# Performance work log

Hardware: AMD Instinct MI355X
Metric: run time of the kernel (lower is better)

## Reference

```python
import jax, jax.numpy as jnp
import numpy as np

B, T, N, IN = 16, 12, 2048, 1
HID, E_DIM, CHEB, HOR = 64, 10, 2, 12


def setup_inputs() -> dict:
    key = jax.random.key(0)
    ks = jax.random.split(key, 12)
    s = 0.1  # param scale to keep gates unsaturated
    return {
        "source": jax.random.normal(ks[0], (B, T, N, IN), jnp.float32),
        "node_embeddings": jax.random.normal(ks[1], (N, E_DIM), jnp.float32),
        "Wg0": jax.random.normal(ks[2], (E_DIM, CHEB, IN + HID, 2 * HID), jnp.float32) * s,
        "bg0": jax.random.normal(ks[3], (E_DIM, 2 * HID), jnp.float32) * s,
        "Wu0": jax.random.normal(ks[4], (E_DIM, CHEB, IN + HID, HID), jnp.float32) * s,
        "bu0": jax.random.normal(ks[5], (E_DIM, HID), jnp.float32) * s,
        "Wg1": jax.random.normal(ks[6], (E_DIM, CHEB, HID + HID, 2 * HID), jnp.float32) * s,
        "bg1": jax.random.normal(ks[7], (E_DIM, 2 * HID), jnp.float32) * s,
        "Wu1": jax.random.normal(ks[8], (E_DIM, CHEB, HID + HID, HID), jnp.float32) * s,
        "bu1": jax.random.normal(ks[9], (E_DIM, HID), jnp.float32) * s,
        "conv_w": jax.random.normal(ks[10], (HOR, HID), jnp.float32) * s,
        "conv_b": jax.random.normal(ks[11], (HOR,), jnp.float32) * s,
    }


def _cheb_supports(E, cheb_k):
    # softmax(relu(E E^T)) row-normalized adaptive adjacency + Chebyshev recursion
    S = jax.nn.softmax(jax.nn.relu(E @ E.T), axis=1)
    sup = [jnp.eye(E.shape[0], dtype=S.dtype), S]
    for _ in range(2, cheb_k):
        sup.append(2.0 * S @ sup[-1] - sup[-2])
    return jnp.stack(sup, axis=0)  # (K, N, N)


def _gcn(x, supports, weights, bias):
    # x: (B,N,C); weights: (N,K,C,O); bias: (N,O)
    x_g = jnp.einsum('knm,bmc->bnkc', supports, x)
    return jnp.einsum('bnki,nkio->bno', x_g, weights) + bias


def _layer(x_seq, supports, E, Wg, bg, Wu, bu, hid):
    # precompute node-adaptive weights/biases (constant across time)
    wg = jnp.einsum('nd,dkio->nkio', E, Wg)
    bgv = E @ bg
    wu = jnp.einsum('nd,dkio->nkio', E, Wu)
    buv = E @ bu

    def step(state, x_t):
        inp = jnp.concatenate([x_t, state], axis=-1)
        zr = jax.nn.sigmoid(_gcn(inp, supports, wg, bgv))
        z, r = jnp.split(zr, 2, axis=-1)
        cand = jnp.concatenate([x_t, z * state], axis=-1)
        hc = jnp.tanh(_gcn(cand, supports, wu, buv))
        h = r * state + (1.0 - r) * hc
        return h, h

    init = jnp.zeros((x_seq.shape[0], x_seq.shape[2], hid), dtype=x_seq.dtype)
    _, hs = jax.lax.scan(step, init, jnp.swapaxes(x_seq, 0, 1))  # (T,B,N,H)
    return jnp.swapaxes(hs, 0, 1)  # (B,T,N,H)


def reference(source, node_embeddings, Wg0, bg0, Wu0, bu0, Wg1, bg1, Wu1, bu1, conv_w, conv_b):
    supports = _cheb_supports(node_embeddings, CHEB)
    h1 = _layer(source, supports, node_embeddings, Wg0, bg0, Wu0, bu0, HID)
    h2 = _layer(h1, supports, node_embeddings, Wg1, bg1, Wu1, bu1, HID)
    last = h2[:, -1]  # (B,N,HID)
    # Conv2d(1, horizon, kernel=(1,HID)) on (B,1,N,HID) == per-node linear over HID
    out = jnp.einsum('bnc,hc->bhn', last, conv_w) + conv_b[None, :, None]
    return out  # (B, horizon, N)
```

## Files before the change

kernel.cpp:

```cpp
#include <hip/hip_runtime.h>
#include <hip/hip_bf16.h>


#define B_    16
#define T_    12
#define N_    2048
#define HID_  64
#define ED_   10
#define HOR_  12
#define BH    (B_*HID_)
#define BT    (B_*T_)

typedef __hip_bfloat16 bf16;
typedef __attribute__((ext_vector_type(8))) short short8;
typedef __attribute__((ext_vector_type(4))) float floatx4;

__device__ __forceinline__ float b2f(bf16 x){ return __bfloat162float(x); }
__device__ __forceinline__ bf16  f2b(float x){ return __float2bfloat16(x); }
__device__ __forceinline__ float bits2f(unsigned u) {
  union { float f; unsigned i; } c; c.i = u << 16; return c.f;
}
__device__ __forceinline__ float ldin(const void* p, size_t i, int isbf) {
  return isbf ? b2f(((const bf16*)p)[i]) : ((const float*)p)[i];
}
__device__ __forceinline__ void fma4(float4& a, float s, const float4& b) {
  a.x += s*b.x; a.y += s*b.y; a.z += s*b.z; a.w += s*b.w;
}

__global__ void k_detect(const void* __restrict__ E, int* __restrict__ flag) {
  __shared__ int cnt;
  if (threadIdx.x == 0) cnt = 0;
  __syncthreads();
  const unsigned* w = (const unsigned*)E;
  int c = 0;
  for (int i = threadIdx.x; i < 4096; i += 256) {
    const unsigned e = (w[i] >> 7) & 0xFFu;
    if (e >= 0x6Eu && e <= 0x86u) ++c;
  }
  atomicAdd(&cnt, c);
  __syncthreads();
  if (threadIdx.x == 0) flag[0] = (cnt > 2048) ? 1 : 0;
}

__global__ void k_castE(const void* __restrict__ E, float* __restrict__ Ein,
                        const int* __restrict__ flag) {
  const int i = blockIdx.x*256 + threadIdx.x;
  if (i < N_*ED_) Ein[i] = ldin(E, i, flag[0]);
}
__global__ void k_castsrc(const void* __restrict__ src, float* __restrict__ srcf,
                          const int* __restrict__ flag) {
  const int i = blockIdx.x*256 + threadIdx.x;
  if (i < B_*T_*N_) srcf[i] = ldin(src, i, flag[0]);
}
__global__ void k_castc(const void* __restrict__ cw, const void* __restrict__ cb,
                        float* __restrict__ cwf, float* __restrict__ cbf,
                        const int* __restrict__ flag) {
  const int i = blockIdx.x*256 + threadIdx.x;
  const int f = flag[0];
  if (i < HOR_*HID_) cwf[i] = ldin(cw, i, f);
  if (i < HOR_)      cbf[i] = ldin(cb, i, f);
}

__global__ __launch_bounds__(256) void k_softmax_S(const float* __restrict__ Ein,
                                                   float* __restrict__ S) {
  const int n = blockIdx.x, tid = threadIdx.x;
  __shared__ float er[ED_];
  __shared__ float red[4];
  if (tid < ED_) er[tid] = Ein[n*ED_ + tid];
  __syncthreads();
  float e[ED_];
#pragma unroll
  for (int d = 0; d < ED_; ++d) e[d] = er[d];
  float v[8];
  float mx = 0.f;
#pragma unroll
  for (int j = 0; j < 8; ++j) {
    const int m = tid + j*256;
    float dot = 0.f;
#pragma unroll
    for (int d = 0; d < ED_; ++d) dot += e[d]*Ein[m*ED_ + d];
    v[j] = fmaxf(dot, 0.f);
    mx = fmaxf(mx, v[j]);
  }
  for (int o = 32; o; o >>= 1) mx = fmaxf(mx, __shfl_xor(mx, o, 64));
  if ((tid & 63) == 0) red[tid >> 6] = mx;
  __syncthreads();
  mx = fmaxf(fmaxf(red[0], red[1]), fmaxf(red[2], red[3]));
  __syncthreads();
  float sum = 0.f;
#pragma unroll
  for (int j = 0; j < 8; ++j) { v[j] = __expf(v[j] - mx); sum += v[j]; }
  for (int o = 32; o; o >>= 1) sum += __shfl_xor(sum, o, 64);
  if ((tid & 63) == 0) red[tid >> 6] = sum;
  __syncthreads();
  sum = red[0] + red[1] + red[2] + red[3];
  const float inv = 1.f / sum;
#pragma unroll
  for (int j = 0; j < 8; ++j)
    S[(size_t)n*N_ + tid + j*256] = v[j]*inv;
}

__global__ void k_splitS(const float* __restrict__ S, bf16* __restrict__ Sh,
                         bf16* __restrict__ Sl, int n) {
  const int i = blockIdx.x*256 + threadIdx.x;
  if (i < n) {
    const float v = S[i];
    const bf16 h = f2b(v);
    Sh[i] = h;
    Sl[i] = f2b(v - b2f(h));
  }
}

__global__ __launch_bounds__(256) void k_trsp(const float* __restrict__ X,
                                              bf16* __restrict__ Th,
                                              bf16* __restrict__ Tl) {
  const int n0 = blockIdx.x * 64;
  const int c0 = blockIdx.y * 64;
  __shared__ float t[64][68];
  const int tid = threadIdx.x;
  {
    const int r = tid >> 2, q4 = (tid & 3) * 16;
    const float4* src = (const float4*)(X + (size_t)(n0 + r)*BH + c0 + q4);
#pragma unroll
    for (int u = 0; u < 4; ++u)
      *(float4*)&t[r][q4 + u*4] = src[u];
  }
  __syncthreads();
  {
    const int c = tid >> 2, sg = (tid & 3) * 16;
    bf16 hb[16], lb[16];
#pragma unroll
    for (int i = 0; i < 16; ++i) {
      const float v = t[sg + i][c];
      const bf16 h = f2b(v);
      hb[i] = h;
      lb[i] = f2b(v - b2f(h));
    }
    bf16* dh = Th + (size_t)(c0 + c)*N_ + n0 + sg;
    bf16* dl = Tl + (size_t)(c0 + c)*N_ + n0 + sg;
    *(uint4*)dh       = *(uint4*)&hb[0];
    *(uint4*)(dh + 8) = *(uint4*)&hb[8];
    *(uint4*)dl       = *(uint4*)&lb[0];
    *(uint4*)(dl + 8) = *(uint4*)&lb[8];
  }
}

template<int LAYER>
__global__ __launch_bounds__(256) void k_prepP(const void* __restrict__ Wb,
                                               float* __restrict__ PF,
                                               bf16* __restrict__ PH,
                                               int KIin, int KIP, int O,
                                               const int* __restrict__ flag) {
  const int idx = blockIdx.x*256 + threadIdx.x;
  if (idx >= ED_*O*KIP) return;
  const int d = idx / (O*KIP), rem = idx - d*O*KIP;
  const int o = rem / KIP, kp = rem - o*KIP;
  int cheb, i; bool valid;
  if (LAYER == 0) {
    cheb = (kp >= 80) ? 1 : 0;
    const int local = kp - cheb*80;
    if (local < 64)       { i = local + 1; valid = true; }
    else if (local == 64) { i = 0;         valid = true; }
    else                  { i = 0;         valid = false; }
  } else {
    cheb = kp >> 7; i = kp & 127; valid = true;
  }
  float v = 0.f;
  if (valid) v = ldin(Wb, (size_t)((d*2 + cheb)*KIin + i)*O + o, flag[0]);
  const int kg = kp >> 2, e = kp & 3;
  const size_t pi = ((size_t)(o*(KIP/4) + kg)*ED_ + d)*4 + e;
  PF[pi] = v;
  PH[pi] = f2b(v);
}

__global__ __launch_bounds__(128) void k_matb(const float* __restrict__ Ein,
                                              const void* __restrict__ bb,
                                              float* __restrict__ outv, int O,
                                              const int* __restrict__ flag) {
  const int n = blockIdx.x, tid = threadIdx.x;
  if (tid >= O) return;
  const int f = flag[0];
  float acc = 0.f;
#pragma unroll
  for (int d = 0; d < ED_; ++d) acc += Ein[n*ED_ + d]*ldin(bb, d*O + tid, f);
  outv[n*O + tid] = acc;
}

__global__ __launch_bounds__(256) void k_gemm64T(const float* __restrict__ S,
                                                 const float* __restrict__ X,
                                                 float* __restrict__ C,
                                                 int ldx, int ldc) {
  const int bm = blockIdx.x * 64;
  const int bc = blockIdx.y * 64;
  __shared__ float St[64][68];
  __shared__ float Xt[64][68];
  const int tid = threadIdx.x;
  const int r0 = (tid >> 4) * 4;
  const int c0 = (tid & 15) * 4;
  float acc[4][4];
#pragma unroll
  for (int i = 0; i < 4; ++i)
#pragma unroll
    for (int j = 0; j < 4; ++j) acc[i][j] = 0.f;
  for (int mk = 0; mk < N_; mk += 64) {
    {
      const int r = tid >> 2, ks = (tid & 3) * 16;
      const float* sp = S + (size_t)(bm + r)*N_ + mk + ks;
#pragma unroll
      for (int u = 0; u < 16; ++u) St[ks + u][r] = sp[u];
      const float* xp = X + (size_t)(bc + r)*ldx + mk + ks;
#pragma unroll
      for (int u = 0; u < 16; ++u) Xt[ks + u][r] = xp[u];
    }
    __syncthreads();
#pragma unroll 4
    for (int kk = 0; kk < 64; ++kk) {
      const float a0 = St[kk][r0], a1 = St[kk][r0+1],
                  a2 = St[kk][r0+2], a3 = St[kk][r0+3];
      const float b0 = Xt[kk][c0], b1 = Xt[kk][c0+1],
                  b2 = Xt[kk][c0+2], b3 = Xt[kk][c0+3];
      acc[0][0] += a0*b0; acc[0][1] += a0*b1; acc[0][2] += a0*b2; acc[0][3] += a0*b3;
      acc[1][0] += a1*b0; acc[1][1] += a1*b1; acc[1][2] += a1*b2; acc[1][3] += a1*b3;
      acc[2][0] += a2*b0; acc[2][1] += a2*b1; acc[2][2] += a2*b2; acc[2][3] += a2*b3;
      acc[3][0] += a3*b0; acc[3][1] += a3*b1; acc[3][2] += a3*b2; acc[3][3] += a3*b3;
    }
    __syncthreads();
  }
#pragma unroll
  for (int i = 0; i < 4; ++i)
#pragma unroll
    for (int j = 0; j < 4; ++j)
      C[(size_t)(bm + r0 + i)*ldc + bc + c0 + j] = acc[i][j];
}

__global__ __launch_bounds__(256) void k_gemmM(const bf16* __restrict__ Sh,
                                               const bf16* __restrict__ Sl,
                                               const bf16* __restrict__ X1h,
                                               const bf16* __restrict__ X1l,
                                               float* __restrict__ C1, int ldc1,
                                               const bf16* __restrict__ X2h,
                                               const bf16* __restrict__ X2l,
                                               float* __restrict__ C2, int ldc2,
                                               int split) {
  const int bm = blockIdx.x * 128;
  int bc = blockIdx.y * 64;
  const bf16* Xh = X1h; const bf16* Xl = X1l; float* C = C1; int ldc = ldc1;
  if (bc >= split) { Xh = X2h; Xl = X2l; C = C2; ldc = ldc2; bc -= split; }

  __shared__ __align__(16) bf16 Ah[128][72];
  __shared__ __align__(16) bf16 Al[128][72];
  __shared__ __align__(16) bf16 Bh[64][72];
  __shared__ __align__(16) bf16 Bl[64][72];
  const int tid = threadIdx.x;
  const int wave = tid >> 6, lane = tid & 63, q = lane >> 4, ln = lane & 15;
  const int wm = wave >> 1, wn = wave & 1;
  const int srow = tid >> 3, scol = (tid & 7) * 8;

  floatx4 acc[4][2];
#pragma unroll
  for (int mt = 0; mt < 4; ++mt)
#pragma unroll
    for (int nt = 0; nt < 2; ++nt) acc[mt][nt] = (floatx4){0.f,0.f,0.f,0.f};

  for (int mk = 0; mk < N_; mk += 64) {
#pragma unroll
    for (int i = 0; i < 4; ++i) {
      const int r = i*32 + srow;
      *(uint4*)&Ah[r][scol] = *(const uint4*)(Sh + (size_t)(bm + r)*N_ + mk + scol);
      *(uint4*)&Al[r][scol] = *(const uint4*)(Sl + (size_t)(bm + r)*N_ + mk + scol);
    }
#pragma unroll
    for (int i = 0; i < 2; ++i) {
      const int r = i*32 + srow;
      *(uint4*)&Bh[r][scol] = *(const uint4*)(Xh + (size_t)(bc + r)*N_ + mk + scol);
      *(uint4*)&Bl[r][scol] = *(const uint4*)(Xl + (size_t)(bc + r)*N_ + mk + scol);
    }
    __syncthreads();
#pragma unroll
    for (int ks = 0; ks < 64; ks += 32) {
      short8 ah[4], al[4], bh[2], bl[2];
#pragma unroll
      for (int mt = 0; mt < 4; ++mt) {
        ah[mt] = *(const short8*)&Ah[wm*64 + mt*16 + ln][ks + q*8];
        al[mt] = *(const short8*)&Al[wm*64 + mt*16 + ln][ks + q*8];
      }
#pragma unroll
      for (int nt = 0; nt < 2; ++nt) {
        bh[nt] = *(const short8*)&Bh[wn*32 + nt*16 + ln][ks + q*8];
        bl[nt] = *(const short8*)&Bl[wn*32 + nt*16 + ln][ks + q*8];
      }
#pragma unroll
      for (int mt = 0; mt < 4; ++mt)
#pragma unroll
        for (int nt = 0; nt < 2; ++nt) {
          acc[mt][nt] = __builtin_amdgcn_mfma_f32_16x16x32_bf16(ah[mt], bh[nt], acc[mt][nt], 0, 0, 0);
          acc[mt][nt] = __builtin_amdgcn_mfma_f32_16x16x32_bf16(al[mt], bh[nt], acc[mt][nt], 0, 0, 0);
          acc[mt][nt] = __builtin_amdgcn_mfma_f32_16x16x32_bf16(ah[mt], bl[nt], acc[mt][nt], 0, 0, 0);
        }
    }
    __syncthreads();
  }
#pragma unroll
  for (int mt = 0; mt < 4; ++mt)
#pragma unroll
    for (int nt = 0; nt < 2; ++nt)
#pragma unroll
      for (int r = 0; r < 4; ++r)
        C[(size_t)(bm + wm*64 + mt*16 + q*4 + r)*ldc + bc + wn*32 + nt*16 + ln] =
            acc[mt][nt][r];
}

template<int LAYER, int KIP, int KIPP>
__device__ __forceinline__ void build4(float (*xg)[KIPP],
                                       const float* p0, const float* p1,
                                       const float* p2, const float* p3,
                                       int n, int t, int tid) {
  constexpr int NQ = KIP/4;
  for (int idx = tid; idx < B_*NQ; idx += 256) {
    const int b = idx / NQ, k = (idx - b*NQ) * 4;
    float4 v = make_float4(0.f, 0.f, 0.f, 0.f);
    if (LAYER == 1) {
      const float* rg = (k < 64) ? p0 : (k < 128) ? p1 : (k < 192) ? p2 : p3;
      v = *(const float4*)(rg + (size_t)n*BH + b*64 + (k & 63));
    } else {
      if (k < 64)        v = *(const float4*)(p0 + (size_t)n*BH + b*64 + k);
      else if (k == 64)  v.x = p1[(size_t)(b*T_ + t)*N_ + n];
      else if (k >= 80 && k < 144)
                         v = *(const float4*)(p2 + (size_t)n*BH + b*64 + (k - 80));
      else if (k == 144) v.x = p3[(size_t)n*BT + b*T_ + t];
    }
    *(float4*)&xg[b][k] = v;
  }
}

template<int KIP>
__device__ __forceinline__ float4 merge_p(const float* __restrict__ PF,
                                          const bf16* __restrict__ PH,
                                          const float* el, int o, int kg,
                                          int isbf) {
  float4 a4 = make_float4(0.f, 0.f, 0.f, 0.f);
  const size_t gbase = (size_t)(o*(KIP/4) + kg)*(ED_*4);
  if (isbf) {
    const uint4* g = (const uint4*)(PH + gbase);
#pragma unroll
    for (int i = 0; i < 5; ++i) {
      const uint4 w = g[i];
      const float e0 = el[2*i], e1 = el[2*i + 1];
      a4.x += e0*bits2f(w.x & 0xFFFFu); a4.y += e0*bits2f(w.x >> 16);
      a4.z += e0*bits2f(w.y & 0xFFFFu); a4.w += e0*bits2f(w.y >> 16);
      a4.x += e1*bits2f(w.z & 0xFFFFu); a4.y += e1*bits2f(w.z >> 16);
      a4.z += e1*bits2f(w.w & 0xFFFFu); a4.w += e1*bits2f(w.w >> 16);
    }
  } else {
    const float4* g = (const float4*)(PF + gbase);
#pragma unroll
    for (int d = 0; d < ED_; ++d)
      fma4(a4, el[d], g[d]);
  }
  return a4;
}

template<int KIP>
__device__ __forceinline__ void merge_p2(const float* __restrict__ PF,
                                         const bf16* __restrict__ PH,
                                         const float* el0, const float* el1,
                                         int o, int kg, int isbf,
                                         float4& a0, float4& a1) {
  const size_t gbase = (size_t)(o*(KIP/4) + kg)*(ED_*4);
  if (isbf) {
    const uint4* g = (const uint4*)(PH + gbase);
#pragma unroll
    for (int i = 0; i < 5; ++i) {
      const uint4 w = g[i];
      const float f0 = bits2f(w.x & 0xFFFFu), f1 = bits2f(w.x >> 16);
      const float f2 = bits2f(w.y & 0xFFFFu), f3 = bits2f(w.y >> 16);
      const float f4 = bits2f(w.z & 0xFFFFu), f5 = bits2f(w.z >> 16);
      const float f6 = bits2f(w.w & 0xFFFFu), f7 = bits2f(w.w >> 16);
      const float e00 = el0[2*i], e01 = el0[2*i + 1];
      const float e10 = el1[2*i], e11 = el1[2*i + 1];
      a0.x += e00*f0; a0.y += e00*f1; a0.z += e00*f2; a0.w += e00*f3;
      a0.x += e01*f4; a0.y += e01*f5; a0.z += e01*f6; a0.w += e01*f7;
      a1.x += e10*f0; a1.y += e10*f1; a1.z += e10*f2; a1.w += e10*f3;
      a1.x += e11*f4; a1.y += e11*f5; a1.z += e11*f6; a1.w += e11*f7;
    }
  } else {
    const float4* g = (const float4*)(PF + gbase);
#pragma unroll
    for (int d = 0; d < ED_; ++d) {
      const float4 w = g[d];
      fma4(a0, el0[d], w);
      fma4(a1, el1[d], w);
    }
  }
}

template<int KIP>
__global__ __launch_bounds__(256) void k_merge(const float* __restrict__ PF,
                                               const bf16* __restrict__ PH,
                                               const float* __restrict__ Ein,
                                               float* __restrict__ WM, int O,
                                               const int* __restrict__ flag) {
  const int n = blockIdx.x;
  const int idx = blockIdx.y*256 + threadIdx.x;
  __shared__ float es[ED_];
  if (threadIdx.x < ED_) es[threadIdx.x] = Ein[n*ED_ + threadIdx.x];
  __syncthreads();
  if (idx >= O*(KIP/4)) return;
  const int o = idx / (KIP/4), kg = idx - o*(KIP/4);
  float el[ED_];
#pragma unroll
  for (int d = 0; d < ED_; ++d) el[d] = es[d];
  const float4 a4 = merge_p<KIP>(PF, PH, el, o, kg, flag[0]);
  *(float4*)&WM[((size_t)n*O + o)*KIP + kg*4] = a4;
}

template<int LAYER, int KIP>
__global__ __launch_bounds__(256, 2) void k_gateWpm(const float* __restrict__ WM,
                                                    const float* __restrict__ bgv,
                                                    const float* __restrict__ p0,
                                                    const float* __restrict__ p1,
                                                    const float* __restrict__ p2,
                                                    const float* __restrict__ p3,
                                                    const float* __restrict__ hstate,
                                                    float* __restrict__ zh,
                                                    float* __restrict__ r_buf,
                                                    int t) {
  constexpr int KIPP = KIP + 4;
  constexpr int O = 128;
  const int n = blockIdx.x, tid = threadIdx.x;
  __shared__ float xg[B_][KIPP];
  __shared__ float wm[O][36];
  build4<LAYER, KIP, KIPP>(xg, p0, p1, p2, p3, n, t, tid);

  const float* WMn = WM + (size_t)n*O*KIP;
  const int b = tid >> 4, q = tid & 15;
  float acc[8];
#pragma unroll
  for (int j = 0; j < 8; ++j) acc[j] = 0.f;

  for (int k0 = 0; k0 < KIP; k0 += 32) {
#pragma unroll
    for (int i = 0; i < O*8/256; ++i) {
      const int idx = tid + i*256;
      const int o = idx >> 3, kq = idx & 7;
      *(float4*)&wm[o][kq*4] =
          *(const float4*)(WMn + (size_t)o*KIP + k0 + kq*4);
    }
    __syncthreads();
#pragma unroll
    for (int kq = 0; kq < 8; ++kq) {
      const float4 xv = *(const float4*)&xg[b][k0 + kq*4];
#pragma unroll
      for (int j = 0; j < 8; ++j) {
        const float4 wv = *(const float4*)&wm[q + 16*j][kq*4];
        acc[j] += xv.x*wv.x + xv.y*wv.y + xv.z*wv.z + xv.w*wv.w;
      }
    }
    __syncthreads();
  }
#pragma unroll
  for (int j = 0; j < 8; ++j) {
    const int o = q + 16*j;
    float s = acc[j] + bgv[n*128 + o];
    s = 1.f/(1.f + __expf(-s));
    if (o < HID_) {
      const float zv = s*hstate[(size_t)n*BH + b*64 + o];
      zh[(size_t)n*BH + b*64 + o] = zv;
    } else {
      r_buf[(size_t)n*BH + b*64 + (o - HID_)] = s;
    }
  }
}

template<int LAYER, int KIP>
__global__ __launch_bounds__(256, 2) void k_candWpm(const float* __restrict__ WM,
                                                    const float* __restrict__ buv,
                                                    const float* __restrict__ p0,
                                                    const float* __restrict__ p1,
                                                    const float* __restrict__ p2,
                                                    const float* __restrict__ p3,
                                                    const float* __restrict__ r_buf,
                                                    float* __restrict__ hstate,
                                                    int t) {
  constexpr int KIPP = KIP + 4;
  constexpr int O = 64;
  const int n = blockIdx.x, tid = threadIdx.x;
  __shared__ float xg[B_][KIPP];
  __shared__ float wm[O][36];
  build4<LAYER, KIP, KIPP>(xg, p0, p1, p2, p3, n, t, tid);

  const float* WMn = WM + (size_t)n*O*KIP;
  const int b = tid >> 4, q = tid & 15;
  float acc[4];
#pragma unroll
  for (int j = 0; j < 4; ++j) acc[j] = 0.f;

  for (int k0 = 0; k0 < KIP; k0 += 32) {
#pragma unroll
    for (int i = 0; i < O*8/256; ++i) {
      const int idx = tid + i*256;
      const int o = idx >> 3, kq = idx & 7;
      *(float4*)&wm[o][kq*4] =
          *(const float4*)(WMn + (size_t)o*KIP + k0 + kq*4);
    }
    __syncthreads();
#pragma unroll
    for (int kq = 0; kq < 8; ++kq) {
      const float4 xv = *(const float4*)&xg[b][k0 + kq*4];
#pragma unroll
      for (int j = 0; j < 4; ++j) {
        const float4 wv = *(const float4*)&wm[q + 16*j][kq*4];
        acc[j] += xv.x*wv.x + xv.y*wv.y + xv.z*wv.z + xv.w*wv.w;
      }
    }
    __syncthreads();
  }
#pragma unroll
  for (int j = 0; j < 4; ++j) {
    const int o = q + 16*j;
    const float hc = tanhf(acc[j] + buv[n*64 + o]);
    const float rr = r_buf[(size_t)n*BH + b*64 + o];
    const float hold = hstate[(size_t)n*BH + b*64 + o];
    const float hn = rr*hold + (1.f - rr)*hc;
    hstate[(size_t)n*BH + b*64 + o] = hn;
  }
}

template<int LAYER, int KIP>
__global__ __launch_bounds__(256, 2) void k_gateW2(const float* __restrict__ PF,
                                                   const bf16* __restrict__ PH,
                                                   const float* __restrict__ bgv,
                                                   const float* __restrict__ p0,
                                                   const float* __restrict__ p1,
                                                   const float* __restrict__ p2,
                                                   const float* __restrict__ p3,
                                                   const float* __restrict__ Ein,
                                                   const float* __restrict__ hstate,
                                                   float* __restrict__ zh,
                                                   float* __restrict__ r_buf,
                                                   const int* __restrict__ flag,
                                                   int t) {
  constexpr int KIPP = KIP + 4;
  constexpr int O = 128;
  const int n0 = blockIdx.x, n1 = blockIdx.x + N_/2, tid = threadIdx.x;
  __shared__ float xg[2][B_][KIPP];
  __shared__ float wm[2][O][36];
  __shared__ float es[2][ED_];
  if (tid < ED_) es[0][tid] = Ein[n0*ED_ + tid];
  if (tid >= 32 && tid < 32 + ED_) es[1][tid - 32] = Ein[n1*ED_ + (tid - 32)];
  build4<LAYER, KIP, KIPP>(xg[0], p0, p1, p2, p3, n0, t, tid);
  build4<LAYER, KIP, KIPP>(xg[1], p0, p1, p2, p3, n1, t, tid);
  __syncthreads();
  const int isbf = flag[0];
  float el0[ED_], el1[ED_];
#pragma unroll
  for (int d = 0; d < ED_; ++d) { el0[d] = es[0][d]; el1[d] = es[1][d]; }

  const int b = tid >> 4, q = tid & 15;
  float ac0[8], ac1[8];
#pragma unroll
  for (int j = 0; j < 8; ++j) { ac0[j] = 0.f; ac1[j] = 0.f; }

  for (int k0 = 0; k0 < KIP; k0 += 32) {
#pragma unroll
    for (int i = 0; i < O*8/256; ++i) {
      const int idx = tid + i*256;
      const int o = idx >> 3, kq = idx & 7;
      float4 a0 = make_float4(0.f, 0.f, 0.f, 0.f);
      float4 a1 = make_float4(0.f, 0.f, 0.f, 0.f);
      merge_p2<KIP>(PF, PH, el0, el1, o, (k0 >> 2) + kq, isbf, a0, a1);
      *(float4*)&wm[0][o][kq*4] = a0;
      *(float4*)&wm[1][o][kq*4] = a1;
    }
    __syncthreads();
#pragma unroll
    for (int kq = 0; kq < 8; ++kq) {
      const float4 xv0 = *(const float4*)&xg[0][b][k0 + kq*4];
      const float4 xv1 = *(const float4*)&xg[1][b][k0 + kq*4];
#pragma unroll
      for (int j = 0; j < 8; ++j) {
        const float4 w0 = *(const float4*)&wm[0][q + 16*j][kq*4];
        const float4 w1 = *(const float4*)&wm[1][q + 16*j][kq*4];
        ac0[j] += xv0.x*w0.x + xv0.y*w0.y + xv0.z*w0.z + xv0.w*w0.w;
        ac1[j] += xv1.x*w1.x + xv1.y*w1.y + xv1.z*w1.z + xv1.w*w1.w;
      }
    }
    __syncthreads();
  }
#pragma unroll
  for (int j = 0; j < 8; ++j) {
    const int o = q + 16*j;
    {
      float s = ac0[j] + bgv[n0*128 + o];
      s = 1.f/(1.f + __expf(-s));
      if (o < HID_) {
        zh[(size_t)n0*BH + b*64 + o] = s*hstate[(size_t)n0*BH + b*64 + o];
      } else {
        r_buf[(size_t)n0*BH + b*64 + (o - HID_)] = s;
      }
    }
    {
      float s = ac1[j] + bgv[n1*128 + o];
      s = 1.f/(1.f + __expf(-s));
      if (o < HID_) {
        zh[(size_t)n1*BH + b*64 + o] = s*hstate[(size_t)n1*BH + b*64 + o];
      } else {
        r_buf[(size_t)n1*BH + b*64 + (o - HID_)] = s;
      }
    }
  }
}

template<int LAYER, int KIP>
__global__ __launch_bounds__(256, 2) void k_candW2f(const float* __restrict__ PF,
                                                    const bf16* __restrict__ PH,
                                                    const float* __restrict__ buv,
                                                    const float* __restrict__ p0,
                                                    const float* __restrict__ p1,
                                                    const float* __restrict__ p2,
                                                    const float* __restrict__ p3,
                                                    const float* __restrict__ Ein,
                                                    const float* __restrict__ r_buf,
                                                    float* __restrict__ hstate,
                                                    const int* __restrict__ flag,
                                                    int t) {
  constexpr int KIPP = KIP + 4;
  constexpr int O = 64;
  const int n0 = blockIdx.x, n1 = blockIdx.x + N_/2, tid = threadIdx.x;
  __shared__ float xg[2][B_][KIPP];
  __shared__ float wm[2][O][36];
  __shared__ float es[2][ED_];
  if (tid < ED_) es[0][tid] = Ein[n0*ED_ + tid];
  if (tid >= 32 && tid < 32 + ED_) es[1][tid - 32] = Ein[n1*ED_ + (tid - 32)];
  build4<LAYER, KIP, KIPP>(xg[0], p0, p1, p2, p3, n0, t, tid);
  build4<LAYER, KIP, KIPP>(xg[1], p0, p1, p2, p3, n1, t, tid);
  __syncthreads();
  const int isbf = flag[0];
  float el0[ED_], el1[ED_];
#pragma unroll
  for (int d = 0; d < ED_; ++d) { el0[d] = es[0][d]; el1[d] = es[1][d]; }

  const int b = tid >> 4, q = tid & 15;
  float ac0[4], ac1[4];
#pragma unroll
  for (int j = 0; j < 4; ++j) { ac0[j] = 0.f; ac1[j] = 0.f; }

  for (int k0 = 0; k0 < KIP; k0 += 32) {
#pragma unroll
    for (int i = 0; i < O*8/256; ++i) {
      const int idx = tid + i*256;
      const int o = idx >> 3, kq = idx & 7;
      float4 a0 = make_float4(0.f, 0.f, 0.f, 0.f);
      float4 a1 = make_float4(0.f, 0.f, 0.f, 0.f);
      merge_p2<KIP>(PF, PH, el0, el1, o, (k0 >> 2) + kq, isbf, a0, a1);
      *(float4*)&wm[0][o][kq*4] = a0;
      *(float4*)&wm[1][o][kq*4] = a1;
    }
    __syncthreads();
#pragma unroll
    for (int kq = 0; kq < 8; ++kq) {
      const float4 xv0 = *(const float4*)&xg[0][b][k0 + kq*4];
      const float4 xv1 = *(const float4*)&xg[1][b][k0 + kq*4];
#pragma unroll
      for (int j = 0; j < 4; ++j) {
        const float4 w0 = *(const float4*)&wm[0][q + 16*j][kq*4];
        const float4 w1 = *(const float4*)&wm[1][q + 16*j][kq*4];
        ac0[j] += xv0.x*w0.x + xv0.y*w0.y + xv0.z*w0.z + xv0.w*w0.w;
        ac1[j] += xv1.x*w1.x + xv1.y*w1.y + xv1.z*w1.z + xv1.w*w1.w;
      }
    }
    __syncthreads();
  }
#pragma unroll
  for (int j = 0; j < 4; ++j) {
    const int o = q + 16*j;
    {
      const float hc = tanhf(ac0[j] + buv[n0*64 + o]);
      const float rr = r_buf[(size_t)n0*BH + b*64 + o];
      const float hold = hstate[(size_t)n0*BH + b*64 + o];
      hstate[(size_t)n0*BH + b*64 + o] = rr*hold + (1.f - rr)*hc;
    }
    {
      const float hc = tanhf(ac1[j] + buv[n1*64 + o]);
      const float rr = r_buf[(size_t)n1*BH + b*64 + o];
      const float hold = hstate[(size_t)n1*BH + b*64 + o];
      hstate[(size_t)n1*BH + b*64 + o] = rr*hold + (1.f - rr)*hc;
    }
  }
}

__global__ void k_zero_f(float* __restrict__ p, int n) {
  const int i = blockIdx.x*256 + threadIdx.x;
  if (i < n) p[i] = 0.f;
}
__global__ void k_zero_out(void* __restrict__ out, int nelem,
                           const int* __restrict__ flag) {
  const int i = blockIdx.x*256 + threadIdx.x;
  if (i < nelem) {
    if (flag[0]) ((unsigned short*)out)[i] = 0;
    else         ((float*)out)[i] = 0.f;
  }
}

__global__ __launch_bounds__(256) void k_conv(const float* __restrict__ h2,
                                              const float* __restrict__ cwf,
                                              const float* __restrict__ cbf,
                                              void* __restrict__ out,
                                              const int* __restrict__ flag) {
  const int n = blockIdx.x, tid = threadIdx.x;
  __shared__ float hs[BH];
  for (int i = tid; i < BH; i += 256) hs[i] = h2[(size_t)n*BH + i];
  __syncthreads();
  const int isbf = flag[0];
  for (int i = tid; i < B_*HOR_; i += 256) {
    const int b = i / HOR_, hor = i - b*HOR_;
    float acc = cbf[hor];
#pragma unroll
    for (int c = 0; c < HID_; ++c) acc += hs[b*HID_ + c]*cwf[hor*HID_ + c];
    const size_t oi = (size_t)(b*HOR_ + hor)*N_ + n;
    if (isbf) ((bf16*)out)[oi] = f2b(acc);
    else      ((float*)out)[oi] = acc;
  }
}

extern "C" void kernel_launch(void* const* d_in, const int* in_sizes, int n_in,
                              void* d_out, int out_size, void* d_ws, size_t ws_size,
                              hipStream_t stream) {
  const void* src = d_in[0];
  const void* E   = d_in[1];
  const void* Wg0 = d_in[2];
  const void* bg0 = d_in[3];
  const void* Wu0 = d_in[4];
  const void* bu0 = d_in[5];
  const void* Wg1 = d_in[6];
  const void* bg1 = d_in[7];
  const void* Wu1 = d_in[8];
  const void* bu1 = d_in[9];
  const void* cw  = d_in[10];
  const void* cb  = d_in[11];
  (void)in_sizes; (void)n_in;

  char* p = (char*)d_ws;
  char* ws_end = (char*)d_ws + ws_size;
  auto alloc = [&](size_t bytes) -> char* {
    char* r = p; p += (bytes + 255) & ~(size_t)255; return r;
  };
  const size_t SL = (size_t)N_*BH;
  int*   flag  = (int*)  alloc(256);
  float* Ein   = (float*)alloc((size_t)N_*ED_*4);
  float* cwf   = (float*)alloc((size_t)HOR_*HID_*4);
  float* cbf   = (float*)alloc((size_t)HOR_*4);
  float* S_f   = (float*)alloc((size_t)N_*N_*4);
  bf16*  S_hi  = (bf16*) alloc((size_t)N_*N_*2);
  bf16*  S_lo  = (bf16*) alloc((size_t)N_*N_*2);
  float* Wg0F  = (float*)alloc((size_t)ED_*128*160*4);
  float* Wu0F  = (float*)alloc((size_t)ED_*64*160*4);
  float* Wg1F  = (float*)alloc((size_t)ED_*128*256*4);
  float* Wu1F  = (float*)alloc((size_t)ED_*64*256*4);
  bf16*  Wg0H  = (bf16*) alloc((size_t)ED_*128*160*2);
  bf16*  Wu0H  = (bf16*) alloc((size_t)ED_*64*160*2);
  bf16*  Wg1H  = (bf16*) alloc((size_t)ED_*128*256*2);
  bf16*  Wu1H  = (bf16*) alloc((size_t)ED_*64*256*2);
  float* bgv0  = (float*)alloc((size_t)N_*128*4);
  float* buv0  = (float*)alloc((size_t)N_*64*4);
  float* bgv1  = (float*)alloc((size_t)N_*128*4);
  float* buv1  = (float*)alloc((size_t)N_*64*4);
  float* srcf  = (float*)alloc((size_t)BT*N_*4);
  float* Sx0   = (float*)alloc((size_t)N_*BT*4);
  float* h0    = (float*)alloc(SL*4);
  float* h2    = (float*)alloc(SL*4);
  float* Sh_a  = (float*)alloc(SL*4);
  float* Sh_b  = (float*)alloc(SL*4);
  float* zh    = (float*)alloc(SL*4);
  float* r_buf = (float*)alloc(SL*4);
  bf16*  zhTh  = (bf16*) alloc(SL*2);
  bf16*  zhTl  = (bf16*) alloc(SL*2);
  bf16*  h0Th  = (bf16*) alloc(SL*2);
  bf16*  h0Tl  = (bf16*) alloc(SL*2);
  bf16*  h2Th  = (bf16*) alloc(SL*2);
  bf16*  h2Tl  = (bf16*) alloc(SL*2);

  const size_t required_base = (size_t)(p - (char*)d_ws);

  float* Wu0M = (float*)alloc((size_t)N_*64*160*4);   bool pmWu0 = (p <= ws_end);
  float* Wu1M = (float*)alloc((size_t)N_*64*256*4);   bool pmWu1 = (p <= ws_end);
  float* Wg0M = (float*)alloc((size_t)N_*128*160*4);  bool pmWg0 = (p <= ws_end);
  float* Wg1M = (float*)alloc((size_t)N_*128*256*4);  bool pmWg1 = (p <= ws_end);

  auto cdiv = [](int a, int b) { return (a + b - 1) / b; };

  k_detect<<<dim3(1), 256, 0, stream>>>(E, flag);

  if (required_base > ws_size) {
    k_zero_out<<<dim3(cdiv(out_size, 256)), 256, 0, stream>>>(d_out, out_size, flag);
    return;
  }

  k_castE  <<<dim3(cdiv(N_*ED_, 256)), 256, 0, stream>>>(E, Ein, flag);
  k_castsrc<<<dim3(cdiv(BT*N_, 256)),  256, 0, stream>>>(src, srcf, flag);
  k_castc  <<<dim3(cdiv(HOR_*HID_, 256)), 256, 0, stream>>>(cw, cb, cwf, cbf, flag);
  k_prepP<0><<<dim3(cdiv(ED_*128*160, 256)), 256, 0, stream>>>(Wg0, Wg0F, Wg0H, 65, 160, 128, flag);
  k_prepP<0><<<dim3(cdiv(ED_*64*160,  256)), 256, 0, stream>>>(Wu0, Wu0F, Wu0H, 65, 160, 64, flag);
  k_prepP<1><<<dim3(cdiv(ED_*128*256, 256)), 256, 0, stream>>>(Wg1, Wg1F, Wg1H, 128, 256, 128, flag);
  k_prepP<1><<<dim3(cdiv(ED_*64*256,  256)), 256, 0, stream>>>(Wu1, Wu1F, Wu1H, 128, 256, 64, flag);
  k_matb<<<dim3(N_), 128, 0, stream>>>(Ein, bg0, bgv0, 128, flag);
  k_matb<<<dim3(N_), 128, 0, stream>>>(Ein, bu0, buv0, 64,  flag);
  k_matb<<<dim3(N_), 128, 0, stream>>>(Ein, bg1, bgv1, 128, flag);
  k_matb<<<dim3(N_), 128, 0, stream>>>(Ein, bu1, buv1, 64,  flag);
  k_softmax_S<<<dim3(N_), 256, 0, stream>>>(Ein, S_f);
  k_splitS<<<dim3(cdiv(N_*N_, 256)), 256, 0, stream>>>(S_f, S_hi, S_lo, N_*N_);

  if (pmWu0) k_merge<160><<<dim3(N_, 10), 256, 0, stream>>>(Wu0F, Wu0H, Ein, Wu0M, 64,  flag);
  if (pmWu1) k_merge<256><<<dim3(N_, 16), 256, 0, stream>>>(Wu1F, Wu1H, Ein, Wu1M, 64,  flag);
  if (pmWg0) k_merge<160><<<dim3(N_, 20), 256, 0, stream>>>(Wg0F, Wg0H, Ein, Wg0M, 128, flag);
  if (pmWg1) k_merge<256><<<dim3(N_, 32), 256, 0, stream>>>(Wg1F, Wg1H, Ein, Wg1M, 128, flag);

  k_gemm64T<<<dim3(N_/64, BT/64), 256, 0, stream>>>(S_f, srcf, Sx0, N_, BT);

  k_zero_f<<<dim3((int)((2*SL + 255)/256)), 256, 0, stream>>>(h0, (int)(2*SL));
  k_zero_f<<<dim3((int)((2*SL + 255)/256)), 256, 0, stream>>>(Sh_a, (int)(2*SL));

  auto run_gate0 = [&](int t) {
    if (pmWg0)
      k_gateWpm<0,160><<<dim3(N_), 256, 0, stream>>>(Wg0M, bgv0, h0, srcf, Sh_a, Sx0,
                                                     h0, zh, r_buf, t);
    else
      k_gateW2<0,160><<<dim3(N_/2), 256, 0, stream>>>(Wg0F, Wg0H, bgv0, h0, srcf, Sh_a, Sx0,
                                                      Ein, h0, zh, r_buf, flag, t);
  };
  auto run_cand0 = [&](int t) {
    if (pmWu0)
      k_candWpm<0,160><<<dim3(N_), 256, 0, stream>>>(Wu0M, buv0, zh, srcf, Sh_b, Sx0,
                                                     r_buf, h0, t);
    else
      k_candW2f<0,160><<<dim3(N_/2), 256, 0, stream>>>(Wu0F, Wu0H, buv0, zh, srcf, Sh_b, Sx0,
                                                       Ein, r_buf, h0, flag, t);
  };
  auto run_gate1 = [&](int t) {
    if (pmWg1)
      k_gateWpm<1,256><<<dim3(N_), 256, 0, stream>>>(Wg1M, bgv1, h0, h2, Sh_a, Sh_b,
                                                     h2, zh, r_buf, t);
    else
      k_gateW2<1,256><<<dim3(N_/2), 256, 0, stream>>>(Wg1F, Wg1H, bgv1, h0, h2, Sh_a, Sh_b,
                                                      Ein, h2, zh, r_buf, flag, t);
  };
  auto run_cand1 = [&](int t) {
    if (pmWu1)
      k_candWpm<1,256><<<dim3(N_), 256, 0, stream>>>(Wu1M, buv1, h0, zh, Sh_a, Sh_b,
                                                     r_buf, h2, t);
    else
      k_candW2f<1,256><<<dim3(N_/2), 256, 0, stream>>>(Wu1F, Wu1H, buv1, h0, zh, Sh_a, Sh_b,
                                                       Ein, r_buf, h2, flag, t);
  };
  auto trsp = [&](const float* X, bf16* Th, bf16* Tl) {
    k_trsp<<<dim3(N_/64, BH/64), 256, 0, stream>>>(X, Th, Tl);
  };

  run_gate0(0);
  run_cand0(0);
  trsp(h0, h0Th, h0Tl);
  k_gemmM<<<dim3(N_/128, BH/64), 256, 0, stream>>>(S_hi, S_lo, h0Th, h0Tl, Sh_a, BH,
                                                   h0Th, h0Tl, Sh_a, BH, 1 << 30);
  run_gate1(0);
  run_cand1(0);
  trsp(h2, h2Th, h2Tl);

  for (int t = 1; t < T_; ++t) {
    run_gate0(t);
    trsp(zh, zhTh, zhTl);
    k_gemmM<<<dim3(N_/128, BH/64), 256, 0, stream>>>(S_hi, S_lo, zhTh, zhTl, Sh_b, BH,
                                                     zhTh, zhTl, Sh_b, BH, 1 << 30);
    run_cand0(t);
    trsp(h0, h0Th, h0Tl);
    k_gemmM<<<dim3(N_/128, 2*BH/64), 256, 0, stream>>>(S_hi, S_lo, h0Th, h0Tl, Sh_a, BH,
                                                       h2Th, h2Tl, Sh_b, BH, BH);
    run_gate1(t);
    trsp(zh, zhTh, zhTl);
    k_gemmM<<<dim3(N_/128, BH/64), 256, 0, stream>>>(S_hi, S_lo, zhTh, zhTl, Sh_b, BH,
                                                     zhTh, zhTl, Sh_b, BH, 1 << 30);
    run_cand1(t);
    trsp(h2, h2Th, h2Tl);
  }

  k_conv<<<dim3(N_), 256, 0, stream>>>(h2, cwf, cbf, d_out, flag);
}
```

Baseline: 5.764 ms.

## Move buffers to static device globals and drop premerged-weight and fp32 GEMM paths

Replaces workspace-allocated buffers with statically sized __device__ globals that kernels select by index arguments, so the code no longer depends on workspace size. It drops the per-node premerged-weight kernels (k_merge, k_gateWpm, k_candWpm) and always uses the on-the-fly merge kernels. The fp32 S matrix and its split pass are removed by having softmax write the bf16 hi/lo parts directly. The fp32 source GEMM is replaced with the split-bf16 MFMA GEMM on pre-split source. It also reorders inputs by matching their byte sizes. This avoids the large merged-weight materialization and the separate split pass, but the premerged path may have been faster per step when enough workspace was available.

```diff
diff --git a/kernel.cpp b/kernel.cpp
--- a/kernel.cpp
+++ b/kernel.cpp
@@ -10,10 +10,42 @@
 #define HOR_  12
 #define BH    (B_*HID_)
 #define BT    (B_*T_)
+#define SL_   (N_*BH)
 
 typedef __hip_bfloat16 bf16;
 typedef __attribute__((ext_vector_type(8))) short short8;
 typedef __attribute__((ext_vector_type(4))) float floatx4;
+
+__device__ int            g_flag[64];
+__device__ float          g_Ein[N_*ED_];
+__device__ float          g_cwf[HOR_*HID_];
+__device__ float          g_cbf[HOR_ + 4];
+__device__ unsigned short g_Shi[N_*N_];
+__device__ unsigned short g_Slo[N_*N_];
+__device__ float          g_Wg0F[ED_*128*160];
+__device__ float          g_Wu0F[ED_*64*160];
+__device__ float          g_Wg1F[ED_*128*256];
+__device__ float          g_Wu1F[ED_*64*256];
+__device__ unsigned short g_Wg0H[ED_*128*160];
+__device__ unsigned short g_Wu0H[ED_*64*160];
+__device__ unsigned short g_Wg1H[ED_*128*256];
+__device__ unsigned short g_Wu1H[ED_*64*256];
+__device__ float          g_bgv0[N_*128];
+__device__ float          g_buv0[N_*64];
+__device__ float          g_bgv1[N_*128];
+__device__ float          g_buv1[N_*64];
+__device__ float          g_srcf[BT*N_];
+__device__ unsigned short g_srcHi[BT*N_];
+__device__ unsigned short g_srcLo[BT*N_];
+__device__ float          g_Sx0[N_*BT];
+__device__ float          g_h[2*SL_];
+__device__ float          g_Sh[2*SL_];
+__device__ float          g_zh[SL_];
+__device__ float          g_rbuf[SL_];
+__device__ unsigned short g_tmpTh[SL_];
+__device__ unsigned short g_tmpTl[SL_];
+__device__ unsigned short g_h2Th[SL_];
+__device__ unsigned short g_h2Tl[SL_];
 
 __device__ __forceinline__ float b2f(bf16 x){ return __bfloat162float(x); }
 __device__ __forceinline__ bf16  f2b(float x){ return __float2bfloat16(x); }
@@ -27,7 +59,7 @@
   a.x += s*b.x; a.y += s*b.y; a.z += s*b.z; a.w += s*b.w;
 }
 
-__global__ void k_detect(const void* __restrict__ E, int* __restrict__ flag) {
+__global__ void k_detect(const void* __restrict__ E) {
   __shared__ int cnt;
   if (threadIdx.x == 0) cnt = 0;
   __syncthreads();
@@ -39,34 +71,31 @@
   }
   atomicAdd(&cnt, c);
   __syncthreads();
-  if (threadIdx.x == 0) flag[0] = (cnt > 2048) ? 1 : 0;
-}
-
-__global__ void k_castE(const void* __restrict__ E, float* __restrict__ Ein,
-                        const int* __restrict__ flag) {
+  if (threadIdx.x == 0) g_flag[0] = (cnt > 2048) ? 1 : 0;
+}
+
+__global__ void k_castE(const void* __restrict__ E) {
   const int i = blockIdx.x*256 + threadIdx.x;
-  if (i < N_*ED_) Ein[i] = ldin(E, i, flag[0]);
-}
-__global__ void k_castsrc(const void* __restrict__ src, float* __restrict__ srcf,
-                          const int* __restrict__ flag) {
+  if (i < N_*ED_) g_Ein[i] = ldin(E, i, g_flag[0]);
+}
+__global__ void k_castsrc(const void* __restrict__ src) {
   const int i = blockIdx.x*256 + threadIdx.x;
-  if (i < B_*T_*N_) srcf[i] = ldin(src, i, flag[0]);
-}
-__global__ void k_castc(const void* __restrict__ cw, const void* __restrict__ cb,
-                        float* __restrict__ cwf, float* __restrict__ cbf,
-                        const int* __restrict__ flag) {
+  if (i < B_*T_*N_) g_srcf[i] = ldin(src, i, g_flag[0]);
+}
+__global__ void k_castc(const void* __restrict__ cw, const void* __restrict__ cb) {
   const int i = blockIdx.x*256 + threadIdx.x;
-  const int f = flag[0];
-  if (i < HOR_*HID_) cwf[i] = ldin(cw, i, f);
-  if (i < HOR_)      cbf[i] = ldin(cb, i, f);
-}
-
-__global__ __launch_bounds__(256) void k_softmax_S(const float* __restrict__ Ein,
-                                                   float* __restrict__ S) {
+  const int f = g_flag[0];
+  if (i < HOR_*HID_) g_cwf[i] = ldin(cw, i, f);
+  if (i < HOR_)      g_cbf[i] = ldin(cb, i, f);
+}
+
+__global__ __launch_bounds__(256) void k_softmax_S() {
+  bf16* Sh = (bf16*)g_Shi;
+  bf16* Sl = (bf16*)g_Slo;
   const int n = blockIdx.x, tid = threadIdx.x;
   __shared__ float er[ED_];
   __shared__ float red[4];
-  if (tid < ED_) er[tid] = Ein[n*ED_ + tid];
+  if (tid < ED_) er[tid] = g_Ein[n*ED_ + tid];
   __syncthreads();
   float e[ED_];
 #pragma unroll
@@ -78,7 +107,7 @@
     const int m = tid + j*256;
     float dot = 0.f;
 #pragma unroll
-    for (int d = 0; d < ED_; ++d) dot += e[d]*Ein[m*ED_ + d];
+    for (int d = 0; d < ED_; ++d) dot += e[d]*g_Ein[m*ED_ + d];
     v[j] = fmaxf(dot, 0.f);
     mx = fmaxf(mx, v[j]);
   }
@@ -96,24 +125,29 @@
   sum = red[0] + red[1] + red[2] + red[3];
   const float inv = 1.f / sum;
 #pragma unroll
-  for (int j = 0; j < 8; ++j)
-    S[(size_t)n*N_ + tid + j*256] = v[j]*inv;
-}
-
-__global__ void k_splitS(const float* __restrict__ S, bf16* __restrict__ Sh,
-                         bf16* __restrict__ Sl, int n) {
+  for (int j = 0; j < 8; ++j) {
+    const float sv = v[j]*inv;
+    const size_t idx = (size_t)n*N_ + tid + j*256;
+    const bf16 h = f2b(sv);
+    Sh[idx] = h;
+    Sl[idx] = f2b(sv - b2f(h));
+  }
+}
+
+__global__ void k_splitSrc() {
   const int i = blockIdx.x*256 + threadIdx.x;
-  if (i < n) {
-    const float v = S[i];
+  if (i < BT*N_) {
+    const float v = g_srcf[i];
     const bf16 h = f2b(v);
-    Sh[i] = h;
-    Sl[i] = f2b(v - b2f(h));
-  }
-}
-
-__global__ __launch_bounds__(256) void k_trsp(const float* __restrict__ X,
-                                              bf16* __restrict__ Th,
-                                              bf16* __restrict__ Tl) {
+    ((bf16*)g_srcHi)[i] = h;
+    ((bf16*)g_srcLo)[i] = f2b(v - b2f(h));
+  }
+}
+
+__global__ __launch_bounds__(256) void k_trsp(int xsel, int dsel) {
+  const float* X = (xsel == 0) ? g_h : (xsel == 1) ? (g_h + SL_) : g_zh;
+  bf16* Th = (bf16*)((dsel == 0) ? g_tmpTh : g_h2Th);
+  bf16* Tl = (bf16*)((dsel == 0) ? g_tmpTl : g_h2Tl);
   const int n0 = blockIdx.x * 64;
   const int c0 = blockIdx.y * 64;
   __shared__ float t[64][68];
@@ -147,10 +181,12 @@
 
 template<int LAYER>
 __global__ __launch_bounds__(256) void k_prepP(const void* __restrict__ Wb,
-                                               float* __restrict__ PF,
-                                               bf16* __restrict__ PH,
                                                int KIin, int KIP, int O,
-                                               const int* __restrict__ flag) {
+                                               int wsel) {
+  float* PF = (wsel == 0) ? g_Wg0F : (wsel == 1) ? g_Wu0F
+            : (wsel == 2) ? g_Wg1F : g_Wu1F;
+  bf16* PH = (bf16*)((wsel == 0) ? g_Wg0H : (wsel == 1) ? g_Wu0H
+            : (wsel == 2) ? g_Wg1H : g_Wu1H);
   const int idx = blockIdx.x*256 + threadIdx.x;
   if (idx >= ED_*O*KIP) return;
   const int d = idx / (O*KIP), rem = idx - d*O*KIP;
@@ -166,86 +202,38 @@
     cheb = kp >> 7; i = kp & 127; valid = true;
   }
   float v = 0.f;
-  if (valid) v = ldin(Wb, (size_t)((d*2 + cheb)*KIin + i)*O + o, flag[0]);
+  if (valid) v = ldin(Wb, (size_t)((d*2 + cheb)*KIin + i)*O + o, g_flag[0]);
   const int kg = kp >> 2, e = kp & 3;
   const size_t pi = ((size_t)(o*(KIP/4) + kg)*ED_ + d)*4 + e;
   PF[pi] = v;
   PH[pi] = f2b(v);
 }
 
-__global__ __launch_bounds__(128) void k_matb(const float* __restrict__ Ein,
-                                              const void* __restrict__ bb,
-                                              float* __restrict__ outv, int O,
-                                              const int* __restrict__ flag) {
+__global__ __launch_bounds__(128) void k_matb(const void* __restrict__ bb,
+                                              int O, int osel) {
+  float* outv = (osel == 0) ? g_bgv0 : (osel == 1) ? g_buv0
+              : (osel == 2) ? g_bgv1 : g_buv1;
   const int n = blockIdx.x, tid = threadIdx.x;
   if (tid >= O) return;
-  const int f = flag[0];
+  const int f = g_flag[0];
   float acc = 0.f;
 #pragma unroll
-  for (int d = 0; d < ED_; ++d) acc += Ein[n*ED_ + d]*ldin(bb, d*O + tid, f);
+  for (int d = 0; d < ED_; ++d) acc += g_Ein[n*ED_ + d]*ldin(bb, d*O + tid, f);
   outv[n*O + tid] = acc;
 }
 
-__global__ __launch_bounds__(256) void k_gemm64T(const float* __restrict__ S,
-                                                 const float* __restrict__ X,
-                                                 float* __restrict__ C,
-                                                 int ldx, int ldc) {
-  const int bm = blockIdx.x * 64;
-  const int bc = blockIdx.y * 64;
-  __shared__ float St[64][68];
-  __shared__ float Xt[64][68];
-  const int tid = threadIdx.x;
-  const int r0 = (tid >> 4) * 4;
-  const int c0 = (tid & 15) * 4;
-  float acc[4][4];
-#pragma unroll
-  for (int i = 0; i < 4; ++i)
-#pragma unroll
-    for (int j = 0; j < 4; ++j) acc[i][j] = 0.f;
-  for (int mk = 0; mk < N_; mk += 64) {
-    {
-      const int r = tid >> 2, ks = (tid & 3) * 16;
-      const float* sp = S + (size_t)(bm + r)*N_ + mk + ks;
-#pragma unroll
-      for (int u = 0; u < 16; ++u) St[ks + u][r] = sp[u];
-      const float* xp = X + (size_t)(bc + r)*ldx + mk + ks;
-#pragma unroll
-      for (int u = 0; u < 16; ++u) Xt[ks + u][r] = xp[u];
-    }
-    __syncthreads();
-#pragma unroll 4
-    for (int kk = 0; kk < 64; ++kk) {
-      const float a0 = St[kk][r0], a1 = St[kk][r0+1],
-                  a2 = St[kk][r0+2], a3 = St[kk][r0+3];
-      const float b0 = Xt[kk][c0], b1 = Xt[kk][c0+1],
-                  b2 = Xt[kk][c0+2], b3 = Xt[kk][c0+3];
-      acc[0][0] += a0*b0; acc[0][1] += a0*b1; acc[0][2] += a0*b2; acc[0][3] += a0*b3;
-      acc[1][0] += a1*b0; acc[1][1] += a1*b1; acc[1][2] += a1*b2; acc[1][3] += a1*b3;
-      acc[2][0] += a2*b0; acc[2][1] += a2*b1; acc[2][2] += a2*b2; acc[2][3] += a2*b3;
-      acc[3][0] += a3*b0; acc[3][1] += a3*b1; acc[3][2] += a3*b2; acc[3][3] += a3*b3;
-    }
-    __syncthreads();
-  }
-#pragma unroll
-  for (int i = 0; i < 4; ++i)
-#pragma unroll
-    for (int j = 0; j < 4; ++j)
-      C[(size_t)(bm + r0 + i)*ldc + bc + c0 + j] = acc[i][j];
-}
-
-__global__ __launch_bounds__(256) void k_gemmM(const bf16* __restrict__ Sh,
-                                               const bf16* __restrict__ Sl,
-                                               const bf16* __restrict__ X1h,
-                                               const bf16* __restrict__ X1l,
-                                               float* __restrict__ C1, int ldc1,
-                                               const bf16* __restrict__ X2h,
-                                               const bf16* __restrict__ X2l,
-                                               float* __restrict__ C2, int ldc2,
+__global__ __launch_bounds__(256) void k_gemmM(int x1, int c1, int ldc1,
+                                               int x2, int c2, int ldc2,
                                                int split) {
+  const bf16* Sh = (const bf16*)g_Shi;
+  const bf16* Sl = (const bf16*)g_Slo;
   const int bm = blockIdx.x * 128;
   int bc = blockIdx.y * 64;
-  const bf16* Xh = X1h; const bf16* Xl = X1l; float* C = C1; int ldc = ldc1;
-  if (bc >= split) { Xh = X2h; Xl = X2l; C = C2; ldc = ldc2; bc -= split; }
+  int xs = x1, cs = c1, ldc = ldc1;
+  if (bc >= split) { xs = x2; cs = c2; ldc = ldc2; bc -= split; }
+  const bf16* Xh = (const bf16*)((xs == 0) ? g_tmpTh : (xs == 1) ? g_h2Th : g_srcHi);
+  const bf16* Xl = (const bf16*)((xs == 0) ? g_tmpTl : (xs == 1) ? g_h2Tl : g_srcLo);
+  float* C = (cs == 0) ? g_Sh : (cs == 1) ? (g_Sh + SL_) : g_Sx0;
 
   __shared__ __align__(16) bf16 Ah[128][72];
   __shared__ __align__(16) bf16 Al[128][72];
@@ -334,33 +322,6 @@
 }
 
 template<int KIP>
-__device__ __forceinline__ float4 merge_p(const float* __restrict__ PF,
-                                          const bf16* __restrict__ PH,
-                                          const float* el, int o, int kg,
-                                          int isbf) {
-  float4 a4 = make_float4(0.f, 0.f, 0.f, 0.f);
-  const size_t gbase = (size_t)(o*(KIP/4) + kg)*(ED_*4);
-  if (isbf) {
-    const uint4* g = (const uint4*)(PH + gbase);
-#pragma unroll
-    for (int i = 0; i < 5; ++i) {
-      const uint4 w = g[i];
-      const float e0 = el[2*i], e1 = el[2*i + 1];
-      a4.x += e0*bits2f(w.x & 0xFFFFu); a4.y += e0*bits2f(w.x >> 16);
-      a4.z += e0*bits2f(w.y & 0xFFFFu); a4.w += e0*bits2f(w.y >> 16);
-      a4.x += e1*bits2f(w.z & 0xFFFFu); a4.y += e1*bits2f(w.z >> 16);
-      a4.z += e1*bits2f(w.w & 0xFFFFu); a4.w += e1*bits2f(w.w >> 16);
-    }
-  } else {
-    const float4* g = (const float4*)(PF + gbase);
-#pragma unroll
-    for (int d = 0; d < ED_; ++d)
-      fma4(a4, el[d], g[d]);
-  }
-  return a4;
-}
-
-template<int KIP>
 __device__ __forceinline__ void merge_p2(const float* __restrict__ PF,
                                          const bf16* __restrict__ PH,
                                          const float* el0, const float* el1,
@@ -394,164 +355,28 @@
   }
 }
 
-template<int KIP>
-__global__ __launch_bounds__(256) void k_merge(const float* __restrict__ PF,
-                                               const bf16* __restrict__ PH,
-                                               const float* __restrict__ Ein,
-                                               float* __restrict__ WM, int O,
-                                               const int* __restrict__ flag) {
-  const int n = blockIdx.x;
-  const int idx = blockIdx.y*256 + threadIdx.x;
-  __shared__ float es[ED_];
-  if (threadIdx.x < ED_) es[threadIdx.x] = Ein[n*ED_ + threadIdx.x];
-  __syncthreads();
-  if (idx >= O*(KIP/4)) return;
-  const int o = idx / (KIP/4), kg = idx - o*(KIP/4);
-  float el[ED_];
-#pragma unroll
-  for (int d = 0; d < ED_; ++d) el[d] = es[d];
-  const float4 a4 = merge_p<KIP>(PF, PH, el, o, kg, flag[0]);
-  *(float4*)&WM[((size_t)n*O + o)*KIP + kg*4] = a4;
-}
-
 template<int LAYER, int KIP>
-__global__ __launch_bounds__(256, 2) void k_gateWpm(const float* __restrict__ WM,
-                                                    const float* __restrict__ bgv,
-                                                    const float* __restrict__ p0,
-                                                    const float* __restrict__ p1,
-                                                    const float* __restrict__ p2,
-                                                    const float* __restrict__ p3,
-                                                    const float* __restrict__ hstate,
-                                                    float* __restrict__ zh,
-                                                    float* __restrict__ r_buf,
-                                                    int t) {
+__global__ __launch_bounds__(256, 2) void k_gateW2(int t) {
   constexpr int KIPP = KIP + 4;
   constexpr int O = 128;
-  const int n = blockIdx.x, tid = threadIdx.x;
-  __shared__ float xg[B_][KIPP];
-  __shared__ float wm[O][36];
-  build4<LAYER, KIP, KIPP>(xg, p0, p1, p2, p3, n, t, tid);
-
-  const float* WMn = WM + (size_t)n*O*KIP;
-  const int b = tid >> 4, q = tid & 15;
-  float acc[8];
-#pragma unroll
-  for (int j = 0; j < 8; ++j) acc[j] = 0.f;
-
-  for (int k0 = 0; k0 < KIP; k0 += 32) {
-#pragma unroll
-    for (int i = 0; i < O*8/256; ++i) {
-      const int idx = tid + i*256;
-      const int o = idx >> 3, kq = idx & 7;
-      *(float4*)&wm[o][kq*4] =
-          *(const float4*)(WMn + (size_t)o*KIP + k0 + kq*4);
-    }
-    __syncthreads();
-#pragma unroll
-    for (int kq = 0; kq < 8; ++kq) {
-      const float4 xv = *(const float4*)&xg[b][k0 + kq*4];
-#pragma unroll
-      for (int j = 0; j < 8; ++j) {
-        const float4 wv = *(const float4*)&wm[q + 16*j][kq*4];
-        acc[j] += xv.x*wv.x + xv.y*wv.y + xv.z*wv.z + xv.w*wv.w;
-      }
-    }
-    __syncthreads();
-  }
-#pragma unroll
-  for (int j = 0; j < 8; ++j) {
-    const int o = q + 16*j;
-    float s = acc[j] + bgv[n*128 + o];
-    s = 1.f/(1.f + __expf(-s));
-    if (o < HID_) {
-      const float zv = s*hstate[(size_t)n*BH + b*64 + o];
-      zh[(size_t)n*BH + b*64 + o] = zv;
-    } else {
-      r_buf[(size_t)n*BH + b*64 + (o - HID_)] = s;
-    }
-  }
-}
-
-template<int LAYER, int KIP>
-__global__ __launch_bounds__(256, 2) void k_candWpm(const float* __restrict__ WM,
-                                                    const float* __restrict__ buv,
-                                                    const float* __restrict__ p0,
-                                                    const float* __restrict__ p1,
-                                                    const float* __restrict__ p2,
-                                                    const float* __restrict__ p3,
-                                                    const float* __restrict__ r_buf,
-                                                    float* __restrict__ hstate,
-                                                    int t) {
-  constexpr int KIPP = KIP + 4;
-  constexpr int O = 64;
-  const int n = blockIdx.x, tid = threadIdx.x;
-  __shared__ float xg[B_][KIPP];
-  __shared__ float wm[O][36];
-  build4<LAYER, KIP, KIPP>(xg, p0, p1, p2, p3, n, t, tid);
-
-  const float* WMn = WM + (size_t)n*O*KIP;
-  const int b = tid >> 4, q = tid & 15;
-  float acc[4];
-#pragma unroll
-  for (int j = 0; j < 4; ++j) acc[j] = 0.f;
-
-  for (int k0 = 0; k0 < KIP; k0 += 32) {
-#pragma unroll
-    for (int i = 0; i < O*8/256; ++i) {
-      const int idx = tid + i*256;
-      const int o = idx >> 3, kq = idx & 7;
-      *(float4*)&wm[o][kq*4] =
-          *(const float4*)(WMn + (size_t)o*KIP + k0 + kq*4);
-    }
-    __syncthreads();
-#pragma unroll
-    for (int kq = 0; kq < 8; ++kq) {
-      const float4 xv = *(const float4*)&xg[b][k0 + kq*4];
-#pragma unroll
-      for (int j = 0; j < 4; ++j) {
-        const float4 wv = *(const float4*)&wm[q + 16*j][kq*4];
-        acc[j] += xv.x*wv.x + xv.y*wv.y + xv.z*wv.z + xv.w*wv.w;
-      }
-    }
-    __syncthreads();
-  }
-#pragma unroll
-  for (int j = 0; j < 4; ++j) {
-    const int o = q + 16*j;
-    const float hc = tanhf(acc[j] + buv[n*64 + o]);
-    const float rr = r_buf[(size_t)n*BH + b*64 + o];
-    const float hold = hstate[(size_t)n*BH + b*64 + o];
-    const float hn = rr*hold + (1.f - rr)*hc;
-    hstate[(size_t)n*BH + b*64 + o] = hn;
-  }
-}
-
-template<int LAYER, int KIP>
-__global__ __launch_bounds__(256, 2) void k_gateW2(const float* __restrict__ PF,
-                                                   const bf16* __restrict__ PH,
-                                                   const float* __restrict__ bgv,
-                                                   const float* __restrict__ p0,
-                                                   const float* __restrict__ p1,
-                                                   const float* __restrict__ p2,
-                                                   const float* __restrict__ p3,
-                                                   const float* __restrict__ Ein,
-                                                   const float* __restrict__ hstate,
-                                                   float* __restrict__ zh,
-                                                   float* __restrict__ r_buf,
-                                                   const int* __restrict__ flag,
-                                                   int t) {
-  constexpr int KIPP = KIP + 4;
-  constexpr int O = 128;
+  const float* PF = (LAYER == 0) ? g_Wg0F : g_Wg1F;
+  const bf16*  PH = (const bf16*)((LAYER == 0) ? g_Wg0H : g_Wg1H);
+  const float* bgv = (LAYER == 0) ? g_bgv0 : g_bgv1;
+  const float* p0 = g_h;
+  const float* p1 = (LAYER == 0) ? g_srcf : (g_h + SL_);
+  const float* p2 = g_Sh;
+  const float* p3 = (LAYER == 0) ? g_Sx0 : (g_Sh + SL_);
+  const float* hstate = (LAYER == 0) ? g_h : (g_h + SL_);
   const int n0 = blockIdx.x, n1 = blockIdx.x + N_/2, tid = threadIdx.x;
   __shared__ float xg[2][B_][KIPP];
   __shared__ float wm[2][O][36];
   __shared__ float es[2][ED_];
-  if (tid < ED_) es[0][tid] = Ein[n0*ED_ + tid];
-  if (tid >= 32 && tid < 32 + ED_) es[1][tid - 32] = Ein[n1*ED_ + (tid - 32)];
+  if (tid < ED_) es[0][tid] = g_Ein[n0*ED_ + tid];
+  if (tid >= 32 && tid < 32 + ED_) es[1][tid - 32] = g_Ein[n1*ED_ + (tid - 32)];
   build4<LAYER, KIP, KIPP>(xg[0], p0, p1, p2, p3, n0, t, tid);
   build4<LAYER, KIP, KIPP>(xg[1], p0, p1, p2, p3, n1, t, tid);
   __syncthreads();
-  const int isbf = flag[0];
+  const int isbf = g_flag[0];
   float el0[ED_], el1[ED_];
 #pragma unroll
   for (int d = 0; d < ED_; ++d) { el0[d] = es[0][d]; el1[d] = es[1][d]; }
@@ -594,48 +419,45 @@
       float s = ac0[j] + bgv[n0*128 + o];
       s = 1.f/(1.f + __expf(-s));
       if (o < HID_) {
-        zh[(size_t)n0*BH + b*64 + o] = s*hstate[(size_t)n0*BH + b*64 + o];
+        g_zh[(size_t)n0*BH + b*64 + o] = s*hstate[(size_t)n0*BH + b*64 + o];
       } else {
-        r_buf[(size_t)n0*BH + b*64 + (o - HID_)] = s;
+        g_rbuf[(size_t)n0*BH + b*64 + (o - HID_)] = s;
       }
     }
     {
       float s = ac1[j] + bgv[n1*128 + o];
       s = 1.f/(1.f + __expf(-s));
       if (o < HID_) {
-        zh[(size_t)n1*BH + b*64 + o] = s*hstate[(size_t)n1*BH + b*64 + o];
+        g_zh[(size_t)n1*BH + b*64 + o] = s*hstate[(size_t)n1*BH + b*64 + o];
       } else {
-        r_buf[(size_t)n1*BH + b*64 + (o - HID_)] = s;
+        g_rbuf[(size_t)n1*BH + b*64 + (o - HID_)] = s;
       }
     }
   }
 }
 
 template<int LAYER, int KIP>
-__global__ __launch_bounds__(256, 2) void k_candW2f(const float* __restrict__ PF,
-                                                    const bf16* __restrict__ PH,
-                                                    const float* __restrict__ buv,
-                                                    const float* __restrict__ p0,
-                                                    const float* __restrict__ p1,
-                                                    const float* __restrict__ p2,
-                                                    const float* __restrict__ p3,
-                                                    const float* __restrict__ Ein,
-                                                    const float* __restrict__ r_buf,
-                                                    float* __restrict__ hstate,
-                                                    const int* __restrict__ flag,
-                                                    int t) {
+__global__ __launch_bounds__(256, 2) void k_candW2f(int t) {
   constexpr int KIPP = KIP + 4;
   constexpr int O = 64;
+  const float* PF = (LAYER == 0) ? g_Wu0F : g_Wu1F;
+  const bf16*  PH = (const bf16*)((LAYER == 0) ? g_Wu0H : g_Wu1H);
+  const float* buv = (LAYER == 0) ? g_buv0 : g_buv1;
+  const float* p0 = (LAYER == 0) ? g_zh : g_h;
+  const float* p1 = (LAYER == 0) ? g_srcf : g_zh;
+  const float* p2 = (LAYER == 0) ? (g_Sh + SL_) : g_Sh;
+  const float* p3 = (LAYER == 0) ? g_Sx0 : (g_Sh + SL_);
+  float* hstate = (LAYER == 0) ? g_h : (g_h + SL_);
   const int n0 = blockIdx.x, n1 = blockIdx.x + N_/2, tid = threadIdx.x;
   __shared__ float xg[2][B_][KIPP];
   __shared__ float wm[2][O][36];
   __shared__ float es[2][ED_];
-  if (tid < ED_) es[0][tid] = Ein[n0*ED_ + tid];
-  if (tid >= 32 && tid < 32 + ED_) es[1][tid - 32] = Ein[n1*ED_ + (tid - 32)];
+  if (tid < ED_) es[0][tid] = g_Ein[n0*ED_ + tid];
+  if (tid >= 32 && tid < 32 + ED_) es[1][tid - 32] = g_Ein[n1*ED_ + (tid - 32)];
   build4<LAYER, KIP, KIPP>(xg[0], p0, p1, p2, p3, n0, t, tid);
   build4<LAYER, KIP, KIPP>(xg[1], p0, p1, p2, p3, n1, t, tid);
   __syncthreads();
-  const int isbf = flag[0];
+  const int isbf = g_flag[0];
   float el0[ED_], el1[ED_];
 #pragma unroll
   for (int d = 0; d < ED_; ++d) { el0[d] = es[0][d]; el1[d] = es[1][d]; }
@@ -676,47 +498,37 @@
     const int o = q + 16*j;
     {
       const float hc = tanhf(ac0[j] + buv[n0*64 + o]);
-      const float rr = r_buf[(size_t)n0*BH + b*64 + o];
+      const float rr = g_rbuf[(size_t)n0*BH + b*64 + o];
       const float hold = hstate[(size_t)n0*BH + b*64 + o];
       hstate[(size_t)n0*BH + b*64 + o] = rr*hold + (1.f - rr)*hc;
     }
     {
       const float hc = tanhf(ac1[j] + buv[n1*64 + o]);
-      const float rr = r_buf[(size_t)n1*BH + b*64 + o];
+      const float rr = g_rbuf[(size_t)n1*BH + b*64 + o];
       const float hold = hstate[(size_t)n1*BH + b*64 + o];
       hstate[(size_t)n1*BH + b*64 + o] = rr*hold + (1.f - rr)*hc;
     }
   }
 }
 
-__global__ void k_zero_f(float* __restrict__ p, int n) {
+__global__ void k_zero_f(int sel) {
+  float* p = (sel == 0) ? g_h : g_Sh;
   const int i = blockIdx.x*256 + threadIdx.x;
-  if (i < n) p[i] = 0.f;
-}
-__global__ void k_zero_out(void* __restrict__ out, int nelem,
-                           const int* __restrict__ flag) {
-  const int i = blockIdx.x*256 + threadIdx.x;
-  if (i < nelem) {
-    if (flag[0]) ((unsigned short*)out)[i] = 0;
-    else         ((float*)out)[i] = 0.f;
-  }
-}
-
-__global__ __launch_bounds__(256) void k_conv(const float* __restrict__ h2,
-                                              const float* __restrict__ cwf,
-                                              const float* __restrict__ cbf,
-                                              void* __restrict__ out,
-                                              const int* __restrict__ flag) {
+  if (i < 2*SL_) p[i] = 0.f;
+}
+
+__global__ __launch_bounds__(256) void k_conv(void* __restrict__ out) {
+  const float* h2 = g_h + SL_;
   const int n = blockIdx.x, tid = threadIdx.x;
   __shared__ float hs[BH];
   for (int i = tid; i < BH; i += 256) hs[i] = h2[(size_t)n*BH + i];
   __syncthreads();
-  const int isbf = flag[0];
+  const int isbf = g_flag[0];
   for (int i = tid; i < B_*HOR_; i += 256) {
     const int b = i / HOR_, hor = i - b*HOR_;
-    float acc = cbf[hor];
-#pragma unroll
-    for (int c = 0; c < HID_; ++c) acc += hs[b*HID_ + c]*cwf[hor*HID_ + c];
+    float acc = g_cbf[hor];
+#pragma unroll
+    for (int c = 0; c < HID_; ++c) acc += hs[b*HID_ + c]*g_cwf[hor*HID_ + c];
     const size_t oi = (size_t)(b*HOR_ + hor)*N_ + n;
     if (isbf) ((bf16*)out)[oi] = f2b(acc);
     else      ((float*)out)[oi] = acc;
@@ -726,161 +538,98 @@
 extern "C" void kernel_launch(void* const* d_in, const int* in_sizes, int n_in,
                               void* d_out, int out_size, void* d_ws, size_t ws_size,
                               hipStream_t stream) {
-  const void* src = d_in[0];
-  const void* E   = d_in[1];
-  const void* Wg0 = d_in[2];
-  const void* bg0 = d_in[3];
-  const void* Wu0 = d_in[4];
-  const void* bu0 = d_in[5];
-  const void* Wg1 = d_in[6];
-  const void* bg1 = d_in[7];
-  const void* Wu1 = d_in[8];
-  const void* bu1 = d_in[9];
-  const void* cw  = d_in[10];
-  const void* cb  = d_in[11];
-  (void)in_sizes; (void)n_in;
-
-  char* p = (char*)d_ws;
-  char* ws_end = (char*)d_ws + ws_size;
-  auto alloc = [&](size_t bytes) -> char* {
-    char* r = p; p += (bytes + 255) & ~(size_t)255; return r;
+  (void)out_size; (void)d_ws; (void)ws_size;
+
+  static const long long cnt[12] = {
+    393216,
+    20480,
+    166400,
+    1280,
+    83200,
+    640,
+    327680,
+    1280,
+    163840,
+    640,
+    768,
+    12
   };
-  const size_t SL = (size_t)N_*BH;
-  int*   flag  = (int*)  alloc(256);
-  float* Ein   = (float*)alloc((size_t)N_*ED_*4);
-  float* cwf   = (float*)alloc((size_t)HOR_*HID_*4);
-  float* cbf   = (float*)alloc((size_t)HOR_*4);
-  float* S_f   = (float*)alloc((size_t)N_*N_*4);
-  bf16*  S_hi  = (bf16*) alloc((size_t)N_*N_*2);
-  bf16*  S_lo  = (bf16*) alloc((size_t)N_*N_*2);
-  float* Wg0F  = (float*)alloc((size_t)ED_*128*160*4);
-  float* Wu0F  = (float*)alloc((size_t)ED_*64*160*4);
-  float* Wg1F  = (float*)alloc((size_t)ED_*128*256*4);
-  float* Wu1F  = (float*)alloc((size_t)ED_*64*256*4);
-  bf16*  Wg0H  = (bf16*) alloc((size_t)ED_*128*160*2);
-  bf16*  Wu0H  = (bf16*) alloc((size_t)ED_*64*160*2);
-  bf16*  Wg1H  = (bf16*) alloc((size_t)ED_*128*256*2);
-  bf16*  Wu1H  = (bf16*) alloc((size_t)ED_*64*256*2);
-  float* bgv0  = (float*)alloc((size_t)N_*128*4);
-  float* buv0  = (float*)alloc((size_t)N_*64*4);
-  float* bgv1  = (float*)alloc((size_t)N_*128*4);
-  float* buv1  = (float*)alloc((size_t)N_*64*4);
-  float* srcf  = (float*)alloc((size_t)BT*N_*4);
-  float* Sx0   = (float*)alloc((size_t)N_*BT*4);
-  float* h0    = (float*)alloc(SL*4);
-  float* h2    = (float*)alloc(SL*4);
-  float* Sh_a  = (float*)alloc(SL*4);
-  float* Sh_b  = (float*)alloc(SL*4);
-  float* zh    = (float*)alloc(SL*4);
-  float* r_buf = (float*)alloc(SL*4);
-  bf16*  zhTh  = (bf16*) alloc(SL*2);
-  bf16*  zhTl  = (bf16*) alloc(SL*2);
-  bf16*  h0Th  = (bf16*) alloc(SL*2);
-  bf16*  h0Tl  = (bf16*) alloc(SL*2);
-  bf16*  h2Th  = (bf16*) alloc(SL*2);
-  bf16*  h2Tl  = (bf16*) alloc(SL*2);
-
-  const size_t required_base = (size_t)(p - (char*)d_ws);
-
-  float* Wu0M = (float*)alloc((size_t)N_*64*160*4);   bool pmWu0 = (p <= ws_end);
-  float* Wu1M = (float*)alloc((size_t)N_*64*256*4);   bool pmWu1 = (p <= ws_end);
-  float* Wg0M = (float*)alloc((size_t)N_*128*160*4);  bool pmWg0 = (p <= ws_end);
-  float* Wg1M = (float*)alloc((size_t)N_*128*256*4);  bool pmWg1 = (p <= ws_end);
+  const void* in[12];
+  bool ok = (n_in == 12) && (in_sizes != nullptr) && (d_in != nullptr);
+  if (ok) {
+    long long mx = 0;
+    for (int i = 0; i < 12; ++i) if ((long long)in_sizes[i] > mx) mx = in_sizes[i];
+    long long scale = mx / 393216LL;
+    if (scale != 1 && scale != 2 && scale != 4) ok = false;
+    if (ok && scale*393216LL != mx) ok = false;
+    bool used[12] = {false,false,false,false,false,false,false,false,false,false,false,false};
+    for (int k = 0; k < 12 && ok; ++k) {
+      int found = -1;
+      for (int i = 0; i < 12; ++i)
+        if (!used[i] && (long long)in_sizes[i] == cnt[k]*scale) { found = i; break; }
+      if (found < 0) ok = false;
+      else { used[found] = true; in[k] = d_in[found]; }
+    }
+  }
+  if (!ok) for (int k = 0; k < 12; ++k) in[k] = d_in[k];
+
+  const void* src = in[0];
+  const void* E   = in[1];
+  const void* Wg0 = in[2];
+  const void* bg0 = in[3];
+  const void* Wu0 = in[4];
+  const void* bu0 = in[5];
+  const void* Wg1 = in[6];
+  const void* bg1 = in[7];
+  const void* Wu1 = in[8];
+  const void* bu1 = in[9];
+  const void* cw  = in[10];
+  const void* cb  = in[11];
 
   auto cdiv = [](int a, int b) { return (a + b - 1) / b; };
 
-  k_detect<<<dim3(1), 256, 0, stream>>>(E, flag);
-
-  if (required_base > ws_size) {
-    k_zero_out<<<dim3(cdiv(out_size, 256)), 256, 0, stream>>>(d_out, out_size, flag);
-    return;
-  }
-
-  k_castE  <<<dim3(cdiv(N_*ED_, 256)), 256, 0, stream>>>(E, Ein, flag);
-  k_castsrc<<<dim3(cdiv(BT*N_, 256)),  256, 0, stream>>>(src, srcf, flag);
-  k_castc  <<<dim3(cdiv(HOR_*HID_, 256)), 256, 0, stream>>>(cw, cb, cwf, cbf, flag);
-  k_prepP<0><<<dim3(cdiv(ED_*128*160, 256)), 256, 0, stream>>>(Wg0, Wg0F, Wg0H, 65, 160, 128, flag);
-  k_prepP<0><<<dim3(cdiv(ED_*64*160,  256)), 256, 0, stream>>>(Wu0, Wu0F, Wu0H, 65, 160, 64, flag);
-  k_prepP<1><<<dim3(cdiv(ED_*128*256, 256)), 256, 0, stream>>>(Wg1, Wg1F, Wg1H, 128, 256, 128, flag);
-  k_prepP<1><<<dim3(cdiv(ED_*64*256,  256)), 256, 0, stream>>>(Wu1, Wu1F, Wu1H, 128, 256, 64, flag);
-  k_matb<<<dim3(N_), 128, 0, stream>>>(Ein, bg0, bgv0, 128, flag);
-  k_matb<<<dim3(N_), 128, 0, stream>>>(Ein, bu0, buv0, 64,  flag);
-  k_matb<<<dim3(N_), 128, 0, stream>>>(Ein, bg1, bgv1, 128, flag);
-  k_matb<<<dim3(N_), 128, 0, stream>>>(Ein, bu1, buv1, 64,  flag);
-  k_softmax_S<<<dim3(N_), 256, 0, stream>>>(Ein, S_f);
-  k_splitS<<<dim3(cdiv(N_*N_, 256)), 256, 0, stream>>>(S_f, S_hi, S_lo, N_*N_);
-
-  if (pmWu0) k_merge<160><<<dim3(N_, 10), 256, 0, stream>>>(Wu0F, Wu0H, Ein, Wu0M, 64,  flag);
-  if (pmWu1) k_merge<256><<<dim3(N_, 16), 256, 0, stream>>>(Wu1F, Wu1H, Ein, Wu1M, 64,  flag);
-  if (pmWg0) k_merge<160><<<dim3(N_, 20), 256, 0, stream>>>(Wg0F, Wg0H, Ein, Wg0M, 128, flag);
-  if (pmWg1) k_merge<256><<<dim3(N_, 32), 256, 0, stream>>>(Wg1F, Wg1H, Ein, Wg1M, 128, flag);
-
-  k_gemm64T<<<dim3(N_/64, BT/64), 256, 0, stream>>>(S_f, srcf, Sx0, N_, BT);
-
-  k_zero_f<<<dim3((int)((2*SL + 255)/256)), 256, 0, stream>>>(h0, (int)(2*SL));
-  k_zero_f<<<dim3((int)((2*SL + 255)/256)), 256, 0, stream>>>(Sh_a, (int)(2*SL));
-
-  auto run_gate0 = [&](int t) {
-    if (pmWg0)
-      k_gateWpm<0,160><<<dim3(N_), 256, 0, stream>>>(Wg0M, bgv0, h0, srcf, Sh_a, Sx0,
-                                                     h0, zh, r_buf, t);
-    else
-      k_gateW2<0,160><<<dim3(N_/2), 256, 0, stream>>>(Wg0F, Wg0H, bgv0, h0, srcf, Sh_a, Sx0,
-                                                      Ein, h0, zh, r_buf, flag, t);
-  };
-  auto run_cand0 = [&](int t) {
-    if (pmWu0)
-      k_candWpm<0,160><<<dim3(N_), 256, 0, stream>>>(Wu0M, buv0, zh, srcf, Sh_b, Sx0,
-                                                     r_buf, h0, t);
-    else
-      k_candW2f<0,160><<<dim3(N_/2), 256, 0, stream>>>(Wu0F, Wu0H, buv0, zh, srcf, Sh_b, Sx0,
-                                                       Ein, r_buf, h0, flag, t);
-  };
-  auto run_gate1 = [&](int t) {
-    if (pmWg1)
-      k_gateWpm<1,256><<<dim3(N_), 256, 0, stream>>>(Wg1M, bgv1, h0, h2, Sh_a, Sh_b,
-                                                     h2, zh, r_buf, t);
-    else
-      k_gateW2<1,256><<<dim3(N_/2), 256, 0, stream>>>(Wg1F, Wg1H, bgv1, h0, h2, Sh_a, Sh_b,
-                                                      Ein, h2, zh, r_buf, flag, t);
-  };
-  auto run_cand1 = [&](int t) {
-    if (pmWu1)
-      k_candWpm<1,256><<<dim3(N_), 256, 0, stream>>>(Wu1M, buv1, h0, zh, Sh_a, Sh_b,
-                                                     r_buf, h2, t);
-    else
-      k_candW2f<1,256><<<dim3(N_/2), 256, 0, stream>>>(Wu1F, Wu1H, buv1, h0, zh, Sh_a, Sh_b,
-                                                       Ein, r_buf, h2, flag, t);
-  };
-  auto trsp = [&](const float* X, bf16* Th, bf16* Tl) {
-    k_trsp<<<dim3(N_/64, BH/64), 256, 0, stream>>>(X, Th, Tl);
-  };
-
-  run_gate0(0);
-  run_cand0(0);
-  trsp(h0, h0Th, h0Tl);
-  k_gemmM<<<dim3(N_/128, BH/64), 256, 0, stream>>>(S_hi, S_lo, h0Th, h0Tl, Sh_a, BH,
-                                                   h0Th, h0Tl, Sh_a, BH, 1 << 30);
-  run_gate1(0);
-  run_cand1(0);
-  trsp(h2, h2Th, h2Tl);
+  k_detect<<<dim3(1), 256, 0, stream>>>(E);
+
+  k_castE  <<<dim3(cdiv(N_*ED_, 256)), 256, 0, stream>>>(E);
+  k_castsrc<<<dim3(cdiv(BT*N_, 256)),  256, 0, stream>>>(src);
+  k_castc  <<<dim3(cdiv(HOR_*HID_, 256)), 256, 0, stream>>>(cw, cb);
+  k_prepP<0><<<dim3(cdiv(ED_*128*160, 256)), 256, 0, stream>>>(Wg0, 65, 160, 128, 0);
+  k_prepP<0><<<dim3(cdiv(ED_*64*160,  256)), 256, 0, stream>>>(Wu0, 65, 160, 64, 1);
+  k_prepP<1><<<dim3(cdiv(ED_*128*256, 256)), 256, 0, stream>>>(Wg1, 128, 256, 128, 2);
+  k_prepP<1><<<dim3(cdiv(ED_*64*256,  256)), 256, 0, stream>>>(Wu1, 128, 256, 64, 3);
+  k_matb<<<dim3(N_), 128, 0, stream>>>(bg0, 128, 0);
+  k_matb<<<dim3(N_), 128, 0, stream>>>(bu0, 64,  1);
+  k_matb<<<dim3(N_), 128, 0, stream>>>(bg1, 128, 2);
+  k_matb<<<dim3(N_), 128, 0, stream>>>(bu1, 64,  3);
+  k_softmax_S<<<dim3(N_), 256, 0, stream>>>();
+  k_splitSrc<<<dim3(cdiv(BT*N_, 256)), 256, 0, stream>>>();
+
+  k_gemmM<<<dim3(N_/128, BT/64), 256, 0, stream>>>(2, 2, BT, 2, 2, BT, 1 << 30);
+
+  k_zero_f<<<dim3((2*SL_ + 255)/256), 256, 0, stream>>>(0);
+  k_zero_f<<<dim3((2*SL_ + 255)/256), 256, 0, stream>>>(1);
+
+  k_gateW2<0,160><<<dim3(N_/2), 256, 0, stream>>>(0);
+  k_candW2f<0,160><<<dim3(N_/2), 256, 0, stream>>>(0);
+  k_trsp<<<dim3(N_/64, BH/64), 256, 0, stream>>>(0, 0);
+  k_gemmM<<<dim3(N_/128, BH/64), 256, 0, stream>>>(0, 0, BH, 0, 0, BH, 1 << 30);
+  k_gateW2<1,256><<<dim3(N_/2), 256, 0, stream>>>(0);
+  k_candW2f<1,256><<<dim3(N_/2), 256, 0, stream>>>(0);
+  k_trsp<<<dim3(N_/64, BH/64), 256, 0, stream>>>(1, 1);
 
   for (int t = 1; t < T_; ++t) {
-    run_gate0(t);
-    trsp(zh, zhTh, zhTl);
-    k_gemmM<<<dim3(N_/128, BH/64), 256, 0, stream>>>(S_hi, S_lo, zhTh, zhTl, Sh_b, BH,
-                                                     zhTh, zhTl, Sh_b, BH, 1 << 30);
-    run_cand0(t);
-    trsp(h0, h0Th, h0Tl);
-    k_gemmM<<<dim3(N_/128, 2*BH/64), 256, 0, stream>>>(S_hi, S_lo, h0Th, h0Tl, Sh_a, BH,
-                                                       h2Th, h2Tl, Sh_b, BH, BH);
-    run_gate1(t);
-    trsp(zh, zhTh, zhTl);
-    k_gemmM<<<dim3(N_/128, BH/64), 256, 0, stream>>>(S_hi, S_lo, zhTh, zhTl, Sh_b, BH,
-                                                     zhTh, zhTl, Sh_b, BH, 1 << 30);
-    run_cand1(t);
-    trsp(h2, h2Th, h2Tl);
-  }
-
-  k_conv<<<dim3(N_), 256, 0, stream>>>(h2, cwf, cbf, d_out, flag);
-}
+    k_gateW2<0,160><<<dim3(N_/2), 256, 0, stream>>>(t);
+    k_trsp<<<dim3(N_/64, BH/64), 256, 0, stream>>>(2, 0);
+    k_gemmM<<<dim3(N_/128, BH/64), 256, 0, stream>>>(0, 1, BH, 0, 1, BH, 1 << 30);
+    k_candW2f<0,160><<<dim3(N_/2), 256, 0, stream>>>(t);
+    k_trsp<<<dim3(N_/64, BH/64), 256, 0, stream>>>(0, 0);
+    k_gemmM<<<dim3(N_/128, 2*BH/64), 256, 0, stream>>>(0, 0, BH, 1, 1, BH, BH);
+    k_gateW2<1,256><<<dim3(N_/2), 256, 0, stream>>>(t);
+    k_trsp<<<dim3(N_/64, BH/64), 256, 0, stream>>>(2, 0);
+    k_gemmM<<<dim3(N_/128, BH/64), 256, 0, stream>>>(0, 1, BH, 0, 1, BH, 1 << 30);
+    k_candW2f<1,256><<<dim3(N_/2), 256, 0, stream>>>(t);
+    k_trsp<<<dim3(N_/64, BH/64), 256, 0, stream>>>(1, 1);
+  }
+
+  k_conv<<<dim3(N_), 256, 0, stream>>>(d_out);
+}
```

New measurement: 6.704 ms. 16.3% more time.
